# Optimization experiments

Measured on AMD Instinct MI355X. Metric: run time of the kernel, lower is better.

## Reference

```python
import jax, jax.numpy as jnp
import numpy as np

MASK_THRED = 1        # init kwarg mask_thred
TRIPLE_WEIGHT = 1.0   # init kwarg triple_weight (scales gradient of shifted branch)
NEG = -1e30
EPS = 1e-8


def setup_inputs() -> dict:
    key = jax.random.key(0)
    k1, k2 = jax.random.split(key)
    x = jax.random.normal(k1, (2, 128, 96, 96), dtype=jnp.float32)
    mask = jax.random.randint(k2, (96, 96), 0, 2, dtype=jnp.int32)
    return {"x": x, "mask": mask}


def reference(x, mask):
    # x: (B, C, H, W); former = x[:, :C//2], latter = x[:, C//2:]
    B, C, H, W = x.shape
    c2 = C // 2
    hw = H * W

    # shift_sz=1, stride=1, mask_thred=1 -> a location is 'masked' iff mask >= 1
    flag = mask.reshape(hw) >= MASK_THRED  # (hw,) True = inside hole

    former, latter = x[:, :c2], x[:, c2:]

    # similarity path is non-differentiable in the original (hard argmax, detached latter)
    lat = jax.lax.stop_gradient(latter).reshape(B, c2, hw).transpose(0, 2, 1)  # (B, hw, c2)
    # original normalizes only the candidate (non-masked) patches (NCC filters)
    lat_n = lat / jnp.maximum(jnp.linalg.norm(lat, axis=-1, keepdims=True), EPS)

    # cross-correlation of every location against every (normalized) candidate
    sim = jnp.einsum('bic,bjc->bij', lat, lat_n)  # (B, hw, hw)
    # only non-masked locations are valid candidates j
    sim = jnp.where(flag[None, None, :], NEG, sim)
    idx = jnp.argmax(sim, axis=-1)  # (B, hw) nearest non-masked neighbor per location

    # shift: copy the FORMER feature from the matched non-masked location
    fmr = former.reshape(B, c2, hw).transpose(0, 2, 1)  # (B, hw, c2)
    gathered = jnp.take_along_axis(fmr, idx[:, :, None], axis=1)  # (B, hw, c2)

    # triple_weight scales only the gradient of the shifted branch (fwd unchanged)
    tw = jnp.float32(TRIPLE_WEIGHT)
    gathered = gathered * tw + jax.lax.stop_gradient(gathered * (1.0 - tw))

    # shifted features only at masked locations, zero elsewhere
    shift = jnp.where(flag[None, :, None], gathered, jnp.float32(0.0))
    shift = shift.transpose(0, 2, 1).reshape(B, c2, H, W)

    # triple: (former, latter, shifted) -> (B, 3*C//2, H, W)
    return jnp.concatenate([former, latter, shift], axis=1)
```

## Files before the change

### kernel.cpp

```cpp
#include <hip/hip_runtime.h>
#include <math.h>

#define HW 9216
#define C2 64
#define NSTRIP 288
#define NCH 16
#define EPSN 1e-8f

typedef _Float16 f16x8  __attribute__((ext_vector_type(8)));
typedef float    f32x16 __attribute__((ext_vector_type(16)));

__global__ void compact_kernel(const int* __restrict__ mask, int* __restrict__ ilist,
                               int* __restrict__ jlist, int* __restrict__ counts) {
    int t = threadIdx.x;
    int base = t * 9;
    unsigned fl = 0; int cnt = 0;
#pragma unroll
    for (int k = 0; k < 9; k++) {
        int f = (mask[base + k] >= 1) ? 1 : 0;
        fl |= (unsigned)f << k;
        cnt += f;
    }
    int lane = t & 63, wave = t >> 6;
    int v = cnt;
#pragma unroll
    for (int off = 1; off < 64; off <<= 1) {
        int u = __shfl_up(v, off, 64);
        if (lane >= off) v += u;
    }
    __shared__ int wsum[16];
    if (lane == 63) wsum[wave] = v;
    __syncthreads();
    int woff = 0;
#pragma unroll
    for (int w = 0; w < 16; w++) if (w < wave) woff += wsum[w];
    int incl = v + woff;
    int excl = incl - cnt;
    int posF = excl, posU = base - excl;
#pragma unroll
    for (int k = 0; k < 9; k++) {
        int p = base + k;
        if ((fl >> k) & 1u) ilist[posF++] = p; else jlist[posU++] = p;
    }
    if (t == 1023) { counts[0] = incl; counts[1] = HW - incl; }
}

__global__ void norm_kernel(const float* __restrict__ x, float* __restrict__ invAll) {
    int t = blockIdx.x * 256 + threadIdx.x;
    int cc = t & 7;
    int pb = t >> 3;
    int b = pb / HW, p = pb - b * HW;
    const float* xl = x + (size_t)(b * 128 + 64) * HW + p;
    float ss = 0.f;
#pragma unroll
    for (int e = 0; e < 8; e++) { float w = xl[(size_t)(cc * 8 + e) * HW]; ss = fmaf(w, w, ss); }
    ss += __shfl_xor(ss, 1, 64);
    ss += __shfl_xor(ss, 2, 64);
    ss += __shfl_xor(ss, 4, 64);
    if (cc == 0) invAll[pb] = 1.0f / fmaxf(sqrtf(ss), EPSN);
}

__global__ void pack_kernel(const float* __restrict__ x, const int* __restrict__ ilist,
                            const int* __restrict__ jlist, const int* __restrict__ counts,
                            const float* __restrict__ invAll,
                            _Float16* __restrict__ aH, _Float16* __restrict__ aL,
                            _Float16* __restrict__ bH, _Float16* __restrict__ bL,
                            unsigned long long* __restrict__ amax) {
    int pslot = blockIdx.x * 256 + threadIdx.x;
    int cc = blockIdx.y;
    int z = blockIdx.z;
    int b = z >> 1, side = z & 1;
    if (side == 0 && cc == 0) amax[(size_t)b * HW + pslot] = 0ull;
    int cnt = counts[side];
    const int* list = side ? jlist : ilist;
    float v[8];
    if (pslot < cnt) {
        int row = list[pslot];
        const float* xl = x + (size_t)(b * 128 + 64) * HW + row;
        float scale = side ? invAll[b * HW + row] : 1.0f;
#pragma unroll
        for (int e = 0; e < 8; e++) v[e] = xl[(size_t)(cc * 8 + e) * HW] * scale;
    } else {
#pragma unroll
        for (int e = 0; e < 8; e++) v[e] = 0.f;
    }
    f16x8 hh, ll;
#pragma unroll
    for (int e = 0; e < 8; e++) {
        float w = v[e];
        _Float16 h = (_Float16)w;
        hh[e] = h;
        ll[e] = (_Float16)((w - (float)h) * 2048.0f);
    }
    int ks = cc >> 1, g = cc & 1;
    int strip = pslot >> 5, ln = pslot & 31;
    size_t off = ((((size_t)b * NSTRIP + strip) * 4 + ks) * 64 + (g * 32 + ln)) * 8;
    _Float16* dh = side ? bH : aH;
    _Float16* dl = side ? bL : aL;
    *(f16x8*)(dh + off) = hh;
    *(f16x8*)(dl + off) = ll;
}

__device__ __forceinline__ unsigned int ordf(float f) {
    unsigned int u = __float_as_uint(f);
    return (u & 0x80000000u) ? ~u : (u | 0x80000000u);
}

__global__ __launch_bounds__(256, 4) void argmax_kernel(
    const _Float16* __restrict__ aH, const _Float16* __restrict__ aL,
    const _Float16* __restrict__ bH, const _Float16* __restrict__ bL,
    const int* __restrict__ ilist, const int* __restrict__ counts,
    unsigned long long* __restrict__ amax)
{
    int ni = counts[0];
    if (blockIdx.x * 128 >= ni) return;
    int nj = counts[1];
    int b = blockIdx.z, s = blockIdx.y;
    int wave = threadIdx.x >> 6, l = threadIdx.x & 63;
    int strip = blockIdx.x * 4 + wave;
    if (strip * 32 >= ni) return;
    int g = l >> 5, ln = l & 31;
    int il = strip * 32 + ln;

    const f16x8* apH = (const f16x8*)aH + ((size_t)b * NSTRIP + strip) * 256 + l;
    const f16x8* apL = (const f16x8*)aL + ((size_t)b * NSTRIP + strip) * 256 + l;
    f16x8 ah0 = apH[0], ah1 = apH[64], ah2 = apH[128], ah3 = apH[192];
    f16x8 al0 = apL[0], al1 = apL[64], al2 = apL[128], al3 = apL[192];

    int njt = (nj + 31) >> 5;
    int tpc = (njt + NCH - 1) / NCH;
    int jt0 = s * tpc, jt1 = min(jt0 + tpc, njt);
    float bestv = -INFINITY; int bestj = -1;
    const f16x8* bpH0 = (const f16x8*)bH + (size_t)b * NSTRIP * 256 + l;
    const f16x8* bpL0 = (const f16x8*)bL + (size_t)b * NSTRIP * 256 + l;

    for (int jt = jt0; jt < jt1; ++jt) {
        const f16x8* bpH = bpH0 + (size_t)jt * 256;
        const f16x8* bpL = bpL0 + (size_t)jt * 256;
        f16x8 bh0 = bpH[0], bh1 = bpH[64], bh2 = bpH[128], bh3 = bpH[192];
        f16x8 bl0 = bpL[0], bl1 = bpL[64], bl2 = bpL[128], bl3 = bpL[192];
        f32x16 accH = {}, accC = {};
        accH = __builtin_amdgcn_mfma_f32_32x32x16_f16(bh0, ah0, accH, 0, 0, 0);
        accC = __builtin_amdgcn_mfma_f32_32x32x16_f16(bh0, al0, accC, 0, 0, 0);
        accC = __builtin_amdgcn_mfma_f32_32x32x16_f16(bl0, ah0, accC, 0, 0, 0);
        accH = __builtin_amdgcn_mfma_f32_32x32x16_f16(bh1, ah1, accH, 0, 0, 0);
        accC = __builtin_amdgcn_mfma_f32_32x32x16_f16(bh1, al1, accC, 0, 0, 0);
        accC = __builtin_amdgcn_mfma_f32_32x32x16_f16(bl1, ah1, accC, 0, 0, 0);
        accH = __builtin_amdgcn_mfma_f32_32x32x16_f16(bh2, ah2, accH, 0, 0, 0);
        accC = __builtin_amdgcn_mfma_f32_32x32x16_f16(bh2, al2, accC, 0, 0, 0);
        accC = __builtin_amdgcn_mfma_f32_32x32x16_f16(bl2, ah2, accC, 0, 0, 0);
        accH = __builtin_amdgcn_mfma_f32_32x32x16_f16(bh3, ah3, accH, 0, 0, 0);
        accC = __builtin_amdgcn_mfma_f32_32x32x16_f16(bh3, al3, accC, 0, 0, 0);
        accC = __builtin_amdgcn_mfma_f32_32x32x16_f16(bl3, ah3, accC, 0, 0, 0);
        int jb = jt << 5;
#pragma unroll
        for (int r = 0; r < 16; ++r) {
            int row = (r & 3) + 8 * (r >> 2) + 4 * g;
            int j = jb + row;
            float vv = fmaf(accC[r], 4.8828125e-4f , accH[r]);
            if (j < nj && vv > bestv) { bestv = vv; bestj = j; }
        }
    }
    unsigned long long key = ((unsigned long long)ordf(bestv) << 32) |
                             (unsigned long long)(~(unsigned int)bestj);
    unsigned long long other = __shfl_xor(key, 32, 64);
    if (other > key) key = other;
    if (g == 0 && il < ni && (unsigned)(key >> 32) > 0x007FFFFFu) {
        atomicMax(&amax[(size_t)b * HW + ilist[il]], key);
    }
}

__global__ void epilogue_kernel(const float4* __restrict__ x4, const float* __restrict__ x,
                                const int* __restrict__ mask,
                                const unsigned long long* __restrict__ amax,
                                const int* __restrict__ jlist, float4* __restrict__ out4) {
    const int q = HW / 4;
    int t = blockIdx.x * blockDim.x + threadIdx.x;
    if (t >= 2 * 192 * q) return;
    int pos4 = t % q;
    int c = (t / q) % 192;
    int b = t / (192 * q);
    if (c < 128) {
        out4[t] = x4[((size_t)b * 128 + c) * q + pos4];
    } else {
        float4 v = make_float4(0.f, 0.f, 0.f, 0.f);
        float* vp = &v.x;
        int pos = pos4 * 4;
        const float* xf = x + (size_t)(b * 128 + (c - 128)) * HW;
#pragma unroll
        for (int k = 0; k < 4; k++) {
            int p = pos + k;
            if (mask[p] >= 1) {
                unsigned long long key = amax[(size_t)b * HW + p];
                int j = 0;
                if (key != 0ull) j = jlist[(int)(~(unsigned int)key)];
                vp[k] = xf[j];
            }
        }
        out4[t] = v;
    }
}

extern "C" void kernel_launch(void* const* d_in, const int* in_sizes, int n_in,
                              void* d_out, int out_size, void* d_ws, size_t ws_size,
                              hipStream_t stream) {
    const float* x = (const float*)d_in[0];
    const int* mask = (const int*)d_in[1];
    float4* out4 = (float4*)d_out;

    char* ws = (char*)d_ws;
    int*   counts = (int*)ws;
    int*   ilist  = (int*)(ws + 128);
    int*   jlist  = (int*)(ws + 36992);
    unsigned long long* amax = (unsigned long long*)(ws + 73856);
    float* invAll = (float*)(ws + 221312);
    _Float16* aH = (_Float16*)(ws + 295040);
    _Float16* aL = (_Float16*)(ws + 295040 + 1 * 2359296);
    _Float16* bH = (_Float16*)(ws + 295040 + 2 * 2359296);
    _Float16* bL = (_Float16*)(ws + 295040 + 3 * 2359296);

    compact_kernel<<<1, 1024, 0, stream>>>(mask, ilist, jlist, counts);
    norm_kernel<<<(2 * HW * 8) / 256, 256, 0, stream>>>(x, invAll);
    {
        dim3 grid(HW / 256, 8, 4);
        pack_kernel<<<grid, 256, 0, stream>>>(x, ilist, jlist, counts, invAll,
                                              aH, aL, bH, bL, amax);
    }
    {
        dim3 grid(NSTRIP / 4, NCH, 2);
        argmax_kernel<<<grid, 256, 0, stream>>>(aH, aL, bH, bL, ilist, counts, amax);
    }
    {
        int n = 2 * 192 * (HW / 4);
        epilogue_kernel<<<(n + 255) / 256, 256, 0, stream>>>((const float4*)x, x, mask,
                                                             amax, jlist, out4);
    }
}
```

Baseline: 109.4 us.

## Process two query strips per wave and scatter-pack via slot map

The argmax kernel now has each wave handle 64 masked query rows, two 32-row strips, against every candidate tile. Each loaded B tile feeds twice as many MFMAs, which halves candidate-tile traffic per unit of work, at the cost of more registers, hence the launch bound drops to 2. The compaction kernel also writes a per-pixel slot map. Packing then reads x in its natural order and scatters into the A or B layouts, so the gathered reads and the doubled side-dimension grid go away. Padding slots are no longer zeroed; the existing i < ni and j < nj guards are relied on to ignore them.

```diff
diff --git a/kernel.cpp b/kernel.cpp
--- a/kernel.cpp
+++ b/kernel.cpp
@@ -11,7 +11,8 @@
 typedef float    f32x16 __attribute__((ext_vector_type(16)));
 
 __global__ void compact_kernel(const int* __restrict__ mask, int* __restrict__ ilist,
-                               int* __restrict__ jlist, int* __restrict__ counts) {
+                               int* __restrict__ jlist, int* __restrict__ slotmap,
+                               int* __restrict__ counts) {
     int t = threadIdx.x;
     int base = t * 9;
     unsigned fl = 0; int cnt = 0;
@@ -40,7 +41,8 @@
 #pragma unroll
     for (int k = 0; k < 9; k++) {
         int p = base + k;
-        if ((fl >> k) & 1u) ilist[posF++] = p; else jlist[posU++] = p;
+        if ((fl >> k) & 1u) { slotmap[p] = posF | 0x80000000; ilist[posF++] = p; }
+        else               { slotmap[p] = posU;              jlist[posU++] = p; }
     }
     if (t == 1023) { counts[0] = incl; counts[1] = HW - incl; }
 }
@@ -60,43 +62,33 @@
     if (cc == 0) invAll[pb] = 1.0f / fmaxf(sqrtf(ss), EPSN);
 }
 
-__global__ void pack_kernel(const float* __restrict__ x, const int* __restrict__ ilist,
-                            const int* __restrict__ jlist, const int* __restrict__ counts,
+__global__ void pack_kernel(const float* __restrict__ x, const int* __restrict__ slotmap,
                             const float* __restrict__ invAll,
                             _Float16* __restrict__ aH, _Float16* __restrict__ aL,
                             _Float16* __restrict__ bH, _Float16* __restrict__ bL,
                             unsigned long long* __restrict__ amax) {
-    int pslot = blockIdx.x * 256 + threadIdx.x;
+    int p = blockIdx.x * 256 + threadIdx.x;
     int cc = blockIdx.y;
-    int z = blockIdx.z;
-    int b = z >> 1, side = z & 1;
-    if (side == 0 && cc == 0) amax[(size_t)b * HW + pslot] = 0ull;
-    int cnt = counts[side];
-    const int* list = side ? jlist : ilist;
-    float v[8];
-    if (pslot < cnt) {
-        int row = list[pslot];
-        const float* xl = x + (size_t)(b * 128 + 64) * HW + row;
-        float scale = side ? invAll[b * HW + row] : 1.0f;
-#pragma unroll
-        for (int e = 0; e < 8; e++) v[e] = xl[(size_t)(cc * 8 + e) * HW] * scale;
-    } else {
-#pragma unroll
-        for (int e = 0; e < 8; e++) v[e] = 0.f;
-    }
+    int b = blockIdx.z;
+    if (cc == 0) amax[(size_t)b * HW + p] = 0ull;
+    int sm = slotmap[p];
+    int flagged = (sm >> 31) & 1;
+    int slot = sm & 0x7fffffff;
+    const float* xl = x + (size_t)(b * 128 + 64) * HW + p;
+    float scale = flagged ? 1.0f : invAll[b * HW + p];
     f16x8 hh, ll;
 #pragma unroll
     for (int e = 0; e < 8; e++) {
-        float w = v[e];
+        float w = xl[(size_t)(cc * 8 + e) * HW] * scale;
         _Float16 h = (_Float16)w;
         hh[e] = h;
         ll[e] = (_Float16)((w - (float)h) * 2048.0f);
     }
     int ks = cc >> 1, g = cc & 1;
-    int strip = pslot >> 5, ln = pslot & 31;
+    int strip = slot >> 5, ln = slot & 31;
     size_t off = ((((size_t)b * NSTRIP + strip) * 4 + ks) * 64 + (g * 32 + ln)) * 8;
-    _Float16* dh = side ? bH : aH;
-    _Float16* dl = side ? bL : aL;
+    _Float16* dh = flagged ? aH : bH;
+    _Float16* dl = flagged ? aL : bL;
     *(f16x8*)(dh + off) = hh;
     *(f16x8*)(dl + off) = ll;
 }
@@ -106,31 +98,34 @@
     return (u & 0x80000000u) ? ~u : (u | 0x80000000u);
 }
 
-__global__ __launch_bounds__(256, 4) void argmax_kernel(
+__global__ __launch_bounds__(256, 2) void argmax_kernel(
     const _Float16* __restrict__ aH, const _Float16* __restrict__ aL,
     const _Float16* __restrict__ bH, const _Float16* __restrict__ bL,
     const int* __restrict__ ilist, const int* __restrict__ counts,
     unsigned long long* __restrict__ amax)
 {
     int ni = counts[0];
-    if (blockIdx.x * 128 >= ni) return;
+    if (blockIdx.x * 256 >= ni) return;
     int nj = counts[1];
     int b = blockIdx.z, s = blockIdx.y;
     int wave = threadIdx.x >> 6, l = threadIdx.x & 63;
-    int strip = blockIdx.x * 4 + wave;
-    if (strip * 32 >= ni) return;
+    int base = (blockIdx.x * 4 + wave) * 64;
+    if (base >= ni) return;
     int g = l >> 5, ln = l & 31;
-    int il = strip * 32 + ln;
-
-    const f16x8* apH = (const f16x8*)aH + ((size_t)b * NSTRIP + strip) * 256 + l;
-    const f16x8* apL = (const f16x8*)aL + ((size_t)b * NSTRIP + strip) * 256 + l;
-    f16x8 ah0 = apH[0], ah1 = apH[64], ah2 = apH[128], ah3 = apH[192];
-    f16x8 al0 = apL[0], al1 = apL[64], al2 = apL[128], al3 = apL[192];
+    int strip0 = base >> 5;
+
+    const f16x8* apH = (const f16x8*)aH + ((size_t)b * NSTRIP + strip0) * 256 + l;
+    const f16x8* apL = (const f16x8*)aL + ((size_t)b * NSTRIP + strip0) * 256 + l;
+    f16x8 xh0 = apH[0],   xh1 = apH[64],  xh2 = apH[128], xh3 = apH[192];
+    f16x8 xl0 = apL[0],   xl1 = apL[64],  xl2 = apL[128], xl3 = apL[192];
+    f16x8 yh0 = apH[256], yh1 = apH[320], yh2 = apH[384], yh3 = apH[448];
+    f16x8 yl0 = apL[256], yl1 = apL[320], yl2 = apL[384], yl3 = apL[448];
 
     int njt = (nj + 31) >> 5;
     int tpc = (njt + NCH - 1) / NCH;
     int jt0 = s * tpc, jt1 = min(jt0 + tpc, njt);
-    float bestv = -INFINITY; int bestj = -1;
+    float bv0 = -INFINITY, bv1 = -INFINITY;
+    int bj0 = -1, bj1 = -1;
     const f16x8* bpH0 = (const f16x8*)bH + (size_t)b * NSTRIP * 256 + l;
     const f16x8* bpL0 = (const f16x8*)bL + (size_t)b * NSTRIP * 256 + l;
 
@@ -139,34 +134,56 @@
         const f16x8* bpL = bpL0 + (size_t)jt * 256;
         f16x8 bh0 = bpH[0], bh1 = bpH[64], bh2 = bpH[128], bh3 = bpH[192];
         f16x8 bl0 = bpL[0], bl1 = bpL[64], bl2 = bpL[128], bl3 = bpL[192];
-        f32x16 accH = {}, accC = {};
-        accH = __builtin_amdgcn_mfma_f32_32x32x16_f16(bh0, ah0, accH, 0, 0, 0);
-        accC = __builtin_amdgcn_mfma_f32_32x32x16_f16(bh0, al0, accC, 0, 0, 0);
-        accC = __builtin_amdgcn_mfma_f32_32x32x16_f16(bl0, ah0, accC, 0, 0, 0);
-        accH = __builtin_amdgcn_mfma_f32_32x32x16_f16(bh1, ah1, accH, 0, 0, 0);
-        accC = __builtin_amdgcn_mfma_f32_32x32x16_f16(bh1, al1, accC, 0, 0, 0);
-        accC = __builtin_amdgcn_mfma_f32_32x32x16_f16(bl1, ah1, accC, 0, 0, 0);
-        accH = __builtin_amdgcn_mfma_f32_32x32x16_f16(bh2, ah2, accH, 0, 0, 0);
-        accC = __builtin_amdgcn_mfma_f32_32x32x16_f16(bh2, al2, accC, 0, 0, 0);
-        accC = __builtin_amdgcn_mfma_f32_32x32x16_f16(bl2, ah2, accC, 0, 0, 0);
-        accH = __builtin_amdgcn_mfma_f32_32x32x16_f16(bh3, ah3, accH, 0, 0, 0);
-        accC = __builtin_amdgcn_mfma_f32_32x32x16_f16(bh3, al3, accC, 0, 0, 0);
-        accC = __builtin_amdgcn_mfma_f32_32x32x16_f16(bl3, ah3, accC, 0, 0, 0);
+        f32x16 cH0 = {}, cC0 = {}, cH1 = {}, cC1 = {};
+        cH0 = __builtin_amdgcn_mfma_f32_32x32x16_f16(bh0, xh0, cH0, 0, 0, 0);
+        cC0 = __builtin_amdgcn_mfma_f32_32x32x16_f16(bh0, xl0, cC0, 0, 0, 0);
+        cC0 = __builtin_amdgcn_mfma_f32_32x32x16_f16(bl0, xh0, cC0, 0, 0, 0);
+        cH0 = __builtin_amdgcn_mfma_f32_32x32x16_f16(bh1, xh1, cH0, 0, 0, 0);
+        cC0 = __builtin_amdgcn_mfma_f32_32x32x16_f16(bh1, xl1, cC0, 0, 0, 0);
+        cC0 = __builtin_amdgcn_mfma_f32_32x32x16_f16(bl1, xh1, cC0, 0, 0, 0);
+        cH0 = __builtin_amdgcn_mfma_f32_32x32x16_f16(bh2, xh2, cH0, 0, 0, 0);
+        cC0 = __builtin_amdgcn_mfma_f32_32x32x16_f16(bh2, xl2, cC0, 0, 0, 0);
+        cC0 = __builtin_amdgcn_mfma_f32_32x32x16_f16(bl2, xh2, cC0, 0, 0, 0);
+        cH0 = __builtin_amdgcn_mfma_f32_32x32x16_f16(bh3, xh3, cH0, 0, 0, 0);
+        cC0 = __builtin_amdgcn_mfma_f32_32x32x16_f16(bh3, xl3, cC0, 0, 0, 0);
+        cC0 = __builtin_amdgcn_mfma_f32_32x32x16_f16(bl3, xh3, cC0, 0, 0, 0);
+        cH1 = __builtin_amdgcn_mfma_f32_32x32x16_f16(bh0, yh0, cH1, 0, 0, 0);
+        cC1 = __builtin_amdgcn_mfma_f32_32x32x16_f16(bh0, yl0, cC1, 0, 0, 0);
+        cC1 = __builtin_amdgcn_mfma_f32_32x32x16_f16(bl0, yh0, cC1, 0, 0, 0);
+        cH1 = __builtin_amdgcn_mfma_f32_32x32x16_f16(bh1, yh1, cH1, 0, 0, 0);
+        cC1 = __builtin_amdgcn_mfma_f32_32x32x16_f16(bh1, yl1, cC1, 0, 0, 0);
+        cC1 = __builtin_amdgcn_mfma_f32_32x32x16_f16(bl1, yh1, cC1, 0, 0, 0);
+        cH1 = __builtin_amdgcn_mfma_f32_32x32x16_f16(bh2, yh2, cH1, 0, 0, 0);
+        cC1 = __builtin_amdgcn_mfma_f32_32x32x16_f16(bh2, yl2, cC1, 0, 0, 0);
+        cC1 = __builtin_amdgcn_mfma_f32_32x32x16_f16(bl2, yh2, cC1, 0, 0, 0);
+        cH1 = __builtin_amdgcn_mfma_f32_32x32x16_f16(bh3, yh3, cH1, 0, 0, 0);
+        cC1 = __builtin_amdgcn_mfma_f32_32x32x16_f16(bh3, yl3, cC1, 0, 0, 0);
+        cC1 = __builtin_amdgcn_mfma_f32_32x32x16_f16(bl3, yh3, cC1, 0, 0, 0);
         int jb = jt << 5;
 #pragma unroll
         for (int r = 0; r < 16; ++r) {
             int row = (r & 3) + 8 * (r >> 2) + 4 * g;
             int j = jb + row;
-            float vv = fmaf(accC[r], 4.8828125e-4f , accH[r]);
-            if (j < nj && vv > bestv) { bestv = vv; bestj = j; }
+            float v0 = fmaf(cC0[r], 4.8828125e-4f , cH0[r]);
+            float v1 = fmaf(cC1[r], 4.8828125e-4f, cH1[r]);
+            if (j < nj && v0 > bv0) { bv0 = v0; bj0 = j; }
+            if (j < nj && v1 > bv1) { bv1 = v1; bj1 = j; }
         }
     }
-    unsigned long long key = ((unsigned long long)ordf(bestv) << 32) |
-                             (unsigned long long)(~(unsigned int)bestj);
-    unsigned long long other = __shfl_xor(key, 32, 64);
-    if (other > key) key = other;
-    if (g == 0 && il < ni && (unsigned)(key >> 32) > 0x007FFFFFu) {
-        atomicMax(&amax[(size_t)b * HW + ilist[il]], key);
+    unsigned long long k0 = ((unsigned long long)ordf(bv0) << 32) |
+                            (unsigned long long)(~(unsigned int)bj0);
+    unsigned long long k1 = ((unsigned long long)ordf(bv1) << 32) |
+                            (unsigned long long)(~(unsigned int)bj1);
+    unsigned long long o0 = __shfl_xor(k0, 32, 64);
+    unsigned long long o1 = __shfl_xor(k1, 32, 64);
+    if (o0 > k0) k0 = o0;
+    if (o1 > k1) k1 = o1;
+    int il0 = base + ln, il1 = base + 32 + ln;
+    if (g == 0) {
+        if (il0 < ni && (unsigned)(k0 >> 32) > 0x007FFFFFu)
+            atomicMax(&amax[(size_t)b * HW + ilist[il0]], k0);
+        if (il1 < ni && (unsigned)(k1 >> 32) > 0x007FFFFFu)
+            atomicMax(&amax[(size_t)b * HW + ilist[il1]], k1);
     }
 }
 
@@ -209,25 +226,25 @@
     float4* out4 = (float4*)d_out;
 
     char* ws = (char*)d_ws;
-    int*   counts = (int*)ws;
-    int*   ilist  = (int*)(ws + 128);
-    int*   jlist  = (int*)(ws + 36992);
-    unsigned long long* amax = (unsigned long long*)(ws + 73856);
-    float* invAll = (float*)(ws + 221312);
-    _Float16* aH = (_Float16*)(ws + 295040);
-    _Float16* aL = (_Float16*)(ws + 295040 + 1 * 2359296);
-    _Float16* bH = (_Float16*)(ws + 295040 + 2 * 2359296);
-    _Float16* bL = (_Float16*)(ws + 295040 + 3 * 2359296);
-
-    compact_kernel<<<1, 1024, 0, stream>>>(mask, ilist, jlist, counts);
+    int*   counts  = (int*)ws;
+    int*   ilist   = (int*)(ws + 128);
+    int*   jlist   = (int*)(ws + 36992);
+    int*   slotmap = (int*)(ws + 73856);
+    unsigned long long* amax = (unsigned long long*)(ws + 110720);
+    float* invAll  = (float*)(ws + 258176);
+    _Float16* aH = (_Float16*)(ws + 331904);
+    _Float16* aL = (_Float16*)(ws + 331904 + 1 * 2359296);
+    _Float16* bH = (_Float16*)(ws + 331904 + 2 * 2359296);
+    _Float16* bL = (_Float16*)(ws + 331904 + 3 * 2359296);
+
+    compact_kernel<<<1, 1024, 0, stream>>>(mask, ilist, jlist, slotmap, counts);
     norm_kernel<<<(2 * HW * 8) / 256, 256, 0, stream>>>(x, invAll);
     {
-        dim3 grid(HW / 256, 8, 4);
-        pack_kernel<<<grid, 256, 0, stream>>>(x, ilist, jlist, counts, invAll,
-                                              aH, aL, bH, bL, amax);
+        dim3 grid(HW / 256, 8, 2);
+        pack_kernel<<<grid, 256, 0, stream>>>(x, slotmap, invAll, aH, aL, bH, bL, amax);
     }
     {
-        dim3 grid(NSTRIP / 4, NCH, 2);
+        dim3 grid(NSTRIP / 8, NCH, 2);
         argmax_kernel<<<grid, 256, 0, stream>>>(aH, aL, bH, bL, ilist, counts, amax);
     }
     {
```

Result: no change. 109.1 us (-0.3%).
